# Optimization experiments

Measured on AMD Instinct MI355X. Metric: run time of the kernel, lower is better.

## Reference

```python
import jax, jax.numpy as jnp
import numpy as np

BN_EPS = 1e-3  # keras BatchNormalization default epsilon


def _conv(x, w):
    # x: [B,H,W,Cin], w: [kh,kw,Cin,Cout], stride 1, SAME padding
    return jax.lax.conv_general_dilated(
        x, w, window_strides=(1, 1), padding='SAME',
        dimension_numbers=('NHWC', 'HWIO', 'NHWC'))


def _bn(x, g, b, m, v):
    return (x - m) * jax.lax.rsqrt(v + BN_EPS) * g + b


def _pam(x, wq, bq, wk, bk, wv, bv, gamma):
    # Position attention: softmax over HW x HW similarity of 1x1-conv q/k.
    B, H, W, C = x.shape
    q = (_conv(x, wq) + bq).reshape(B, H * W, -1)   # [B,HW,C/8]
    k = (_conv(x, wk) + bk).reshape(B, H * W, -1)   # [B,HW,C/8]
    v = (_conv(x, wv) + bv).reshape(B, H * W, C)    # [B,HW,C]
    energy = jnp.einsum('bic,bjc->bij', q, k)       # [B,HW,HW]
    att = jax.nn.softmax(energy, axis=-1)
    out = jnp.einsum('bij,bjc->bic', att, v).reshape(B, H, W, C)
    return gamma * out + x


def _cam(x, gamma):
    # Channel attention with max-subtract stabilization, softmax over C.
    B, H, W, C = x.shape
    X = x.reshape(B, H * W, C)                      # channel-last flat
    energy = jnp.einsum('bnc,bnd->bcd', X, X)       # [B,C,C]
    energy_new = jnp.max(energy, axis=-1, keepdims=True) - energy
    att = jax.nn.softmax(energy_new, axis=-1)       # [B,C,C]
    out = jnp.einsum('bcd,bnd->bnc', att, X).reshape(B, H, W, C)
    return gamma * out + x


def setup_inputs() -> dict:
    key = jax.random.key(0)
    ks = jax.random.split(key, 16)
    B, H, W = 4, 64, 64
    Cin, Ci, Cq, Cout = 512, 128, 16, 19
    s = 0.05
    d = {
        'x': jax.random.normal(ks[0], (B, H, W, Cin), jnp.float32),
        'w5a': jax.random.normal(ks[1], (3, 3, Cin, Ci), jnp.float32) * s,
        'w5c': jax.random.normal(ks[2], (3, 3, Cin, Ci), jnp.float32) * s,
        'wq': jax.random.normal(ks[3], (1, 1, Ci, Cq), jnp.float32) * s,
        'bq': jnp.zeros((Cq,), jnp.float32),
        'wk': jax.random.normal(ks[4], (1, 1, Ci, Cq), jnp.float32) * s,
        'bk': jnp.zeros((Cq,), jnp.float32),
        'wv': jax.random.normal(ks[5], (1, 1, Ci, Ci), jnp.float32) * s,
        'bv': jnp.zeros((Ci,), jnp.float32),
        'pam_gamma': jnp.float32(0.5),
        'cam_gamma': jnp.float32(0.5),
        'w51': jax.random.normal(ks[6], (3, 3, Ci, Ci), jnp.float32) * s,
        'w52': jax.random.normal(ks[7], (3, 3, Ci, Ci), jnp.float32) * s,
        'w8': jax.random.normal(ks[8], (1, 1, Ci, Cout), jnp.float32) * s,
    }
    for i, nm in enumerate(['bn1', 'bn2', 'bn3', 'bn4']):
        d[nm + '_g'] = jnp.ones((Ci,), jnp.float32)
        d[nm + '_b'] = jnp.zeros((Ci,), jnp.float32)
        d[nm + '_m'] = jax.random.normal(ks[9 + i], (Ci,), jnp.float32) * 0.1
        d[nm + '_v'] = jnp.ones((Ci,), jnp.float32)
    return d


def reference(x, w5a, w5c, wq, bq, wk, bk, wv, bv, pam_gamma, cam_gamma,
              w51, w52, w8,
              bn1_g, bn1_b, bn1_m, bn1_v,
              bn2_g, bn2_b, bn2_m, bn2_v,
              bn3_g, bn3_b, bn3_m, bn3_v,
              bn4_g, bn4_b, bn4_m, bn4_v):
    # PAM branch
    feat1 = jax.nn.relu(_bn(_conv(x, w5a), bn1_g, bn1_b, bn1_m, bn1_v))
    sa_feat = _pam(feat1, wq, bq, wk, bk, wv, bv, pam_gamma)
    sa_conv = jax.nn.relu(_bn(_conv(sa_feat, w51), bn3_g, bn3_b, bn3_m, bn3_v))
    # CAM branch
    feat2 = jax.nn.relu(_bn(_conv(x, w5c), bn2_g, bn2_b, bn2_m, bn2_v))
    sc_feat = _cam(feat2, cam_gamma)
    sc_conv = jax.nn.relu(_bn(_conv(sc_feat, w52), bn4_g, bn4_b, bn4_m, bn4_v))
    # Fused output (dropout is identity at inference)
    feat_sum = sa_conv + sc_conv
    return _conv(feat_sum, w8)
```

## Files before the change

kernel.cpp:

```cpp
#include <hip/hip_runtime.h>
#include <hip/hip_bf16.h>
#include <math.h>

#define BN_EPS 1e-3f
#define LOG2E 1.44269504088896f

constexpr int Bn = 4, Hn = 64, Wn = 64, CIN = 512, CI = 128;
constexpr int HWn = Hn * Wn;
constexpr int NPIX = Bn * HWn;
constexpr int COn = 19;
constexpr int XSL = 66;
constexpr int XPG = XSL * 16;

struct F8 { float4 lo, hi; };

__device__ __forceinline__ F8 f8zero() {
    F8 r; r.lo = make_float4(0.f,0.f,0.f,0.f); r.hi = make_float4(0.f,0.f,0.f,0.f); return r;
}
__device__ __forceinline__ void fma8(F8 &acc, float a, const float4 &wlo, const float4 &whi) {
    acc.lo.x = fmaf(a, wlo.x, acc.lo.x);
    acc.lo.y = fmaf(a, wlo.y, acc.lo.y);
    acc.lo.z = fmaf(a, wlo.z, acc.lo.z);
    acc.lo.w = fmaf(a, wlo.w, acc.lo.w);
    acc.hi.x = fmaf(a, whi.x, acc.hi.x);
    acc.hi.y = fmaf(a, whi.y, acc.hi.y);
    acc.hi.z = fmaf(a, whi.z, acc.hi.z);
    acc.hi.w = fmaf(a, whi.w, acc.hi.w);
}

typedef __attribute__((ext_vector_type(8)))  short    short8;
typedef __attribute__((ext_vector_type(8)))  _Float16 half8;
typedef __attribute__((ext_vector_type(16))) float    f32x16;

__device__ __forceinline__ f32x16 f16z() {
    f32x16 z;
    #pragma unroll
    for (int i = 0; i < 16; ++i) z[i] = 0.f;
    return z;
}
__device__ __forceinline__ unsigned f2b(float f) {
    union { float f; unsigned u; } c; c.f = f;
    return (c.u + 0x7FFFu + ((c.u >> 16) & 1u)) >> 16;
}
__device__ __forceinline__ unsigned pack2(float lo, float hi) {
    return (f2b(hi) << 16) | f2b(lo);
}
__device__ __forceinline__ unsigned pkb2(float a, float b) {
    __hip_bfloat16 ha = __float2bfloat16(a);
    __hip_bfloat16 hb = __float2bfloat16(b);
    return ((unsigned)*(unsigned short*)&hb << 16) | *(unsigned short*)&ha;
}
__device__ __forceinline__ void split2(float a, float b, unsigned &hi, unsigned &lo) {
    const unsigned ha = f2b(a), hb = f2b(b);
    union { unsigned u; float f; } ua, ub; ua.u = ha << 16; ub.u = hb << 16;
    hi = (hb << 16) | ha;
    lo = pack2(a - ua.f, b - ub.f);
}
__device__ __forceinline__ unsigned pkh2(float a, float b) {
    union { _Float16 h; unsigned short u; } ca, cb;
    ca.h = (_Float16)a; cb.h = (_Float16)b;
    return ((unsigned)cb.u << 16) | ca.u;
}

__global__ __launch_bounds__(256)
void k_prep_w(const float* __restrict__ w5a, const float* __restrict__ w5c,
              const float* __restrict__ w51, const float* __restrict__ w52,
              char* __restrict__ wt1F, char* __restrict__ wt2aF, char* __restrict__ wt2bF)
{
    int idx = blockIdx.x * 256 + threadIdx.x;
    if (idx < 589824) {
        const int jp = idx & 7, co = (idx >> 3) & 255, ct = idx >> 11;
        const int tap = ct % 9, c = ct / 9;
        const float* src = (co < 128) ? w5a : w5c;
        const int coc = co & 127;
        const int ci = c*16 + jp*2;
        const float a = src[((size_t)tap*CIN + ci)*CI + coc];
        const float b = src[((size_t)tap*CIN + ci + 1)*CI + coc];
        const int L = co*32 + jp*4;
        *(unsigned*)(wt1F + (size_t)ct*8192 + L) = pkh2(a, b);
    } else {
        int k = idx - 589824;
        if (k >= 147456) return;
        const float* src = (k < 73728) ? w51 : w52;
        char* dstF = (k < 73728) ? wt2aF : wt2bF;
        if (k >= 73728) k -= 73728;
        const int jp = k & 7, co = (k >> 3) & 127, ct = k >> 10;
        const int tap = ct % 9, c = ct / 9;
        const int ci = c*16 + jp*2;
        const float a = src[((size_t)tap*CI + ci)*CI + co];
        const float b = src[((size_t)tap*CI + ci + 1)*CI + co];
        const int L = co*32 + jp*4;
        *(unsigned*)(dstF + (size_t)ct*4096 + L) = pkh2(a, b);
    }
}

__global__ __launch_bounds__(256)
void k_prep_bn(const float* g1, const float* b1, const float* m1, const float* v1,
               const float* g2, const float* b2, const float* m2, const float* v2,
               const float* g3, const float* b3, const float* m3, const float* v3,
               const float* g4, const float* b4, const float* m4, const float* v4,
               float* bnAs, float* bnAb, float* bnBs, float* bnBb)
{
    const int t = threadIdx.x, c = t & 127;
    {
        const float *g = (t < 128) ? g1 : g2, *b = (t < 128) ? b1 : b2;
        const float *m = (t < 128) ? m1 : m2, *v = (t < 128) ? v1 : v2;
        const float s = g[c] * rsqrtf(v[c] + BN_EPS);
        bnAs[t] = s; bnAb[t] = b[c] - m[c]*s;
    }
    {
        const float *g = (t < 128) ? g3 : g4, *b = (t < 128) ? b3 : b4;
        const float *m = (t < 128) ? m3 : m4, *v = (t < 128) ? v3 : v4;
        const float s = g[c] * rsqrtf(v[c] + BN_EPS);
        bnBs[t] = s; bnBb[t] = b[c] - m[c]*s;
    }
}

__global__ __launch_bounds__(256)
void k_prep_x(const float* __restrict__ x, _Float16* __restrict__ xcv)
{
    __shared__ float Xl[16*520];
    const int t = threadIdx.x;
    const int pb = blockIdx.x * 16;
    #pragma unroll
    for (int i = 0; i < 8; ++i) {
        const int u = t + i*256;
        const int px = u >> 7, c4 = (u & 127) * 4;
        *(float4*)&Xl[px*520 + c4] = *(const float4*)&x[(size_t)(pb + px)*CIN + c4];
    }
    __syncthreads();
    const int rowg = pb >> 6, pixb = pb & 63;
    #pragma unroll
    for (int i = 0; i < 8; ++i) {
        const int u = t + i*256;
        const int chunk = u >> 6, rem = u & 63;
        const int pl = rem >> 2, u4 = rem & 3;
        const float* src = &Xl[pl*520 + chunk*16 + u4*4];
        uint2 v;
        v.x = pkh2(src[0], src[1]);
        v.y = pkh2(src[2], src[3]);
        *(uint2*)&xcv[(((size_t)rowg*32 + chunk)*XSL + (pixb + pl + 1))*16 + u4*4] = v;
    }
    if (pixb == 0 && t < 64) {
        const int chunk = t >> 1, sl = (t & 1) * 65;
        uint4* dst = (uint4*)&xcv[(((size_t)rowg*32 + chunk)*XSL + sl)*16];
        uint4 z; z.x = 0u; z.y = 0u; z.z = 0u; z.w = 0u;
        dst[0] = z; dst[1] = z;
    }
}

__global__ __launch_bounds__(256)
void k_zhalo(_Float16* __restrict__ saf_h, _Float16* __restrict__ scf_h)
{
    const int idx = blockIdx.x * 256 + threadIdx.x;
    if (idx >= 8192) return;
    _Float16* arr = (idx & 4096) ? scf_h : saf_h;
    const int rem = idx & 4095;
    const int row = rem >> 4, chunk = (rem >> 1) & 7, sl = (rem & 1) * 65;
    uint4* dst = (uint4*)&arr[(((size_t)row*8 + chunk)*XSL + sl)*16];
    uint4 z; z.x = 0u; z.y = 0u; z.z = 0u; z.w = 0u;
    dst[0] = z; dst[1] = z;
}

template<int NCHNK, int NCOTOT, int WCOBASE>
__global__ __launch_bounds__(512)
void k_convr(const _Float16* __restrict__ xcv0, const _Float16* __restrict__ xcv1,
             const _Float16* __restrict__ wtF0, const _Float16* __restrict__ wtF1,
             const float* __restrict__ bnS, const float* __restrict__ bnBi,
             float* __restrict__ out0, float* __restrict__ out1)
{
    constexpr int WU4  = 1152;
    constexpr int XU4  = 792;
    constexpr int BUFB = (WU4 + XU4) * 16;
    __shared__ __align__(16) char Ls[2*BUFB];

    const int t     = threadIdx.x;
    const int wgid  = blockIdx.x;
    const int slice = wgid & 3;
    const int rg    = wgid >> 2;
    const int sel   = slice >> 1;
    const int ch2   = slice & 1;
    const _Float16* xcv = sel ? xcv1 : xcv0;
    const _Float16* wtF = sel ? wtF1 : wtF0;
    float* dst = sel ? out1 : out0;

    const int hh0 = (rg*4) & 63;
    const int l = t & 63, w = t >> 6;
    const int lo5 = l & 31, hf = l >> 5;
    const int r = w >> 1, mi = w & 1;
    const int cobase0 = WCOBASE*sel + ch2*64;

    bool sAct[4]; bool sIsW[4]; int sDst[4]; size_t sSrc[4]; unsigned sStr[4];
    #pragma unroll
    for (int i = 0; i < 4; ++i) {
        const int u = t + i*512;
        sAct[i] = false; sIsW[i] = false; sDst[i] = -1; sSrc[i] = 0; sStr[i] = 0;
        if (u < WU4) {
            const int tap = u >> 7, rem = u & 127;
            const int co = rem >> 1, whf = rem & 1;
            sAct[i] = true; sIsW[i] = true;
            sSrc[i] = (size_t)(tap*NCOTOT + cobase0 + co)*32 + whf*16;
            sStr[i] = (unsigned)(9*NCOTOT*32);
            sDst[i] = (tap*128 + whf*64 + co) * 16;
        } else if (u < WU4 + XU4) {
            const int j = u - WU4;
            const int page = j / 132, rem132 = j - page*132;
            const int slot = rem132 >> 1, xhf = rem132 & 1;
            const int hin = hh0 + page - 1;
            sAct[i] = (hin >= 0 && hin < Hn);
            const int gr = rg*4 + page - 1;
            sSrc[i] = (size_t)gr*NCHNK*2112 + (size_t)(slot*32 + xhf*16);
            sStr[i] = 2112u;
            sDst[i] = WU4*16 + page*2112 + ((slot*32 + xhf*16) ^ ((slot & 7) << 4));
        }
    }
    int xoff[3][3];
    #pragma unroll
    for (int dy = 0; dy < 3; ++dy)
        #pragma unroll
        for (int dx = 0; dx < 3; ++dx) {
            const int s = mi*32 + lo5 + dx;
            xoff[dy][dx] = WU4*16 + (r + dy)*2112 + ((s*32 + hf*16) ^ ((s & 7) << 4));
        }

    f32x16 acc[2];
    acc[0] = f16z(); acc[1] = f16z();

    uint4 xr[4];
    auto loadS = [&](int c) {
        #pragma unroll
        for (int i = 0; i < 4; ++i) {
            uint4 v; v.x = 0u; v.y = 0u; v.z = 0u; v.w = 0u;
            if (sAct[i]) {
                const char* base = sIsW[i] ? (const char*)wtF : (const char*)xcv;
                v = *(const uint4*)(base + sSrc[i] + (size_t)c*sStr[i]);
            }
            xr[i] = v;
        }
    };

    loadS(0);
    int p = 0;
    for (int c = 0; c < NCHNK; ++c) {
        char* Lp = Ls + p*BUFB;
        #pragma unroll
        for (int i = 0; i < 4; ++i)
            if (sDst[i] >= 0) *(uint4*)(Lp + sDst[i]) = xr[i];
        __syncthreads();
        if (c + 1 < NCHNK) loadS(c + 1);
        #pragma unroll
        for (int dy = 0; dy < 3; ++dy)
            #pragma unroll
            for (int dx = 0; dx < 3; ++dx) {
                const half8 xf = *(const half8*)(Lp + xoff[dy][dx]);
                const half8 w0 = *(const half8*)(Lp + ((dy*3 + dx)*128 + hf*64 + lo5)*16);
                const half8 w1 = *(const half8*)(Lp + ((dy*3 + dx)*128 + hf*64 + 32 + lo5)*16);
                acc[0] = __builtin_amdgcn_mfma_f32_32x32x16_f16(w0, xf, acc[0], 0, 0, 0);
                acc[1] = __builtin_amdgcn_mfma_f32_32x32x16_f16(w1, xf, acc[1], 0, 0, 0);
            }
        p ^= 1;
    }
    const int px = mi*32 + lo5;
    const size_t pg = (size_t)(rg*4 + r)*Wn + px;
    #pragma unroll
    for (int cot = 0; cot < 2; ++cot)
        #pragma unroll
        for (int rr = 0; rr < 16; ++rr) {
            const int crow = (rr & 3) + 8*(rr >> 2) + 4*hf;
            const int och = ch2*64 + cot*32 + crow;
            const int bnidx = sel*128 + och;
            dst[pg*CI + och] = fmaxf(fmaf(acc[cot][rr], bnS[bnidx], bnBi[bnidx]), 0.f);
        }
}

__global__ __launch_bounds__(256)
void k_qk(const float* __restrict__ feat1,
          const float* __restrict__ wq, const float* __restrict__ bq,
          const float* __restrict__ wk, const float* __restrict__ bk,
          __hip_bfloat16* __restrict__ qb, __hip_bfloat16* __restrict__ kb)
{
    __shared__ float Al[64*129];
    __shared__ __align__(16) float Wl[128*32];
    const int t = threadIdx.x;
    const int pb = blockIdx.x * 64;
    for (int idx = t; idx < 64*128; idx += 256) {
        const int p = idx >> 7, ci = idx & 127;
        Al[p*129 + ci] = feat1[(size_t)(pb + p)*CI + ci];
    }
    for (int idx = t; idx < 128*32; idx += 256) {
        const int ci = idx >> 5, c = idx & 31;
        Wl[idx] = (c < 16) ? wq[ci*16 + c] : wk[ci*16 + (c - 16)];
    }
    __syncthreads();
    const int p = t & 63, cg = t >> 6, co = cg * 8;
    F8 acc = f8zero();
    #pragma unroll 8
    for (int ci = 0; ci < 128; ++ci) {
        const float a = Al[p*129 + ci];
        const float4 wlo = *(const float4*)&Wl[ci*32 + co];
        const float4 whi = *(const float4*)&Wl[ci*32 + co + 4];
        fma8(acc, a, wlo, whi);
    }
    const float* af = (const float*)&acc;
    #pragma unroll
    for (int j = 0; j < 8; ++j) {
        const int c = co + j;
        if (c < 16) qb[(size_t)(pb + p)*16 + c]        = __float2bfloat16((af[j] + bq[c]) * LOG2E);
        else        kb[(size_t)(pb + p)*16 + (c - 16)] = __float2bfloat16(af[j] + bk[c - 16]);
    }
}

__global__ __launch_bounds__(256)
void k_v(const float* __restrict__ feat1, const float* __restrict__ wv,
         const float* __restrict__ bv, __hip_bfloat16* __restrict__ vbT)
{
    __shared__ float Al[32*129];
    __shared__ __align__(16) float Wl[64*128];
    const int t = threadIdx.x;
    const int pb = blockIdx.x * 32;
    for (int idx = t; idx < 32*128; idx += 256) {
        const int p = idx >> 7, ci = idx & 127;
        Al[p*129 + ci] = feat1[(size_t)(pb + p)*CI + ci];
    }
    const int px = t & 15, co = (t >> 4) * 8;
    F8 acc0 = f8zero(), acc1 = f8zero();
    for (int ch = 0; ch < 2; ++ch) {
        __syncthreads();
        #pragma unroll
        for (int r = 0; r < 8; ++r) {
            const int i4 = t + r*256;
            const int kk = i4 >> 5, c4 = (i4 & 31) * 4;
            *(float4*)&Wl[kk*128 + c4] = *(const float4*)&wv[(size_t)(ch*64 + kk)*CI + c4];
        }
        __syncthreads();
        #pragma unroll 4
        for (int kk = 0; kk < 64; ++kk) {
            const float a0 = Al[px*129 + ch*64 + kk];
            const float a1 = Al[(px+16)*129 + ch*64 + kk];
            const float4 wlo = *(const float4*)&Wl[kk*128 + co];
            const float4 whi = *(const float4*)&Wl[kk*128 + co + 4];
            fma8(acc0, a0, wlo, whi);
            fma8(acc1, a1, wlo, whi);
        }
    }
    const int p0 = pb + px;
    const int bb = p0 / HWn, pin0 = p0 % HWn;
    const int k16a = pin0 >> 4, ko = pin0 & 15;
    const float* a0f = (const float*)&acc0;
    const float* a1f = (const float*)&acc1;
    #pragma unroll
    for (int j = 0; j < 8; ++j) {
        const int c = co + j;
        const size_t base = ((size_t)bb*256*CI*16) + (size_t)c*16 + ko;
        vbT[base + (size_t)k16a*CI*16]       = __float2bfloat16(a0f[j] + bv[c]);
        vbT[base + (size_t)(k16a + 1)*CI*16] = __float2bfloat16(a1f[j] + bv[c]);
    }
}

__global__ __launch_bounds__(256)
void k_pam(const __hip_bfloat16* __restrict__ qb, const __hip_bfloat16* __restrict__ kb,
           const __hip_bfloat16* __restrict__ vbT, const float* __restrict__ feat1,
           const float* __restrict__ gamma, _Float16* __restrict__ saf_h)
{
    __shared__ __align__(16) char pbuf[16896];
    __shared__ float msArr[4][32];
    __shared__ float ssArr[4][32];
    __shared__ float ssum[32];
    const int t  = threadIdx.x;
    const int wv = t >> 6, l = t & 63;
    const int lo5 = l & 31, h = l >> 5;
    unsigned* Ppk = (unsigned*)(pbuf + wv*4096);
    float* osum = (float*)pbuf;

    const int wgid = blockIdx.x;
    const int xcd  = wgid & 7;
    const int bb   = xcd >> 1;
    const int qt   = ((wgid >> 3) << 1) | (xcd & 1);
    const int q0   = bb*HWn + qt*32;
    const size_t jb = (size_t)bb * HWn;
    const __hip_bfloat16* vbB = vbT + (size_t)bb * 256 * CI * 16;

    const short8 qfrag = *(const short8*)&qb[(size_t)(q0 + lo5)*16 + 8*h];
    const f32x16 zro = f16z();

    f32x16 o[4];
    #pragma unroll
    for (int cb = 0; cb < 4; ++cb) o[cb] = f16z();

    float m_run = -1e30f, s_run = 0.f;

    const int kbeg = wv*1024, kend = kbeg + 1024;
    short8 kf0 = *(const short8*)&kb[(jb + kbeg +      lo5)*16 + 8*h];
    short8 kf1 = *(const short8*)&kb[(jb + kbeg + 32 + lo5)*16 + 8*h];

    for (int k0 = kbeg; k0 < kend; k0 += 64) {
        short8 vf[4][4];
        #pragma unroll
        for (int s = 0; s < 4; ++s)
            #pragma unroll
            for (int cb = 0; cb < 4; ++cb)
                vf[s][cb] = *(const short8*)&vbB[
                    (((size_t)(k0 >> 4) + s)*CI + cb*32 + lo5)*16 + 8*h];

        f32x16 e0 = __builtin_amdgcn_mfma_f32_32x32x16_bf16(kf0, qfrag, zro, 0, 0, 0);
        f32x16 e1 = __builtin_amdgcn_mfma_f32_32x32x16_bf16(kf1, qfrag, zro, 0, 0, 0);

        if (k0 + 64 < kend) {
            kf0 = *(const short8*)&kb[(jb + k0 + 64 +      lo5)*16 + 8*h];
            kf1 = *(const short8*)&kb[(jb + k0 + 64 + 32 + lo5)*16 + 8*h];
        }

        float mx8[8];
        #pragma unroll
        for (int r = 0; r < 8; ++r)
            mx8[r] = fmaxf(fmaxf(e0[r], e0[r+8]), fmaxf(e1[r], e1[r+8]));
        mx8[0] = fmaxf(mx8[0], mx8[4]);
        mx8[1] = fmaxf(mx8[1], mx8[5]);
        mx8[2] = fmaxf(mx8[2], mx8[6]);
        mx8[3] = fmaxf(mx8[3], mx8[7]);
        mx8[0] = fmaxf(mx8[0], mx8[2]);
        mx8[1] = fmaxf(mx8[1], mx8[3]);
        float mt = fmaxf(mx8[0], mx8[1]);
        mt = fmaxf(mt, __shfl_xor(mt, 32));

        if (__any(mt > m_run + 11.5416f)) {
            const float mnew = fmaxf(m_run, mt);
            const float sc = exp2f(m_run - mnew);
            s_run *= sc;
            #pragma unroll
            for (int cb = 0; cb < 4; ++cb)
                #pragma unroll
                for (int r = 0; r < 16; ++r) o[cb][r] *= sc;
            m_run = mnew;
        }

        #pragma unroll
        for (int r = 0; r < 16; ++r) {
            e0[r] = exp2f(e0[r] - m_run);
            e1[r] = exp2f(e1[r] - m_run);
        }
        {
            float s8[8];
            #pragma unroll
            for (int r = 0; r < 8; ++r)
                s8[r] = (e0[r] + e0[r+8]) + (e1[r] + e1[r+8]);
            s8[0] += s8[4]; s8[1] += s8[5]; s8[2] += s8[6]; s8[3] += s8[7];
            s8[0] += s8[2]; s8[1] += s8[3];
            s_run += s8[0] + s8[1];
        }

        #pragma unroll
        for (int r = 0; r < 16; r += 2) {
            const int pidx = ((r & 3) >> 1) + 4*(r >> 2) + 2*h;
            Ppk[pidx*32 + lo5]        = pkb2(e0[r], e0[r+1]);
            Ppk[(16 + pidx)*32 + lo5] = pkb2(e1[r], e1[r+1]);
        }
        #pragma unroll
        for (int s = 0; s < 4; ++s) {
            union { unsigned u[4]; short8 s8; } P;
            #pragma unroll
            for (int w = 0; w < 4; ++w)
                P.u[w] = Ppk[(s*8 + 4*h + w)*32 + lo5];
            #pragma unroll
            for (int cb = 0; cb < 4; ++cb)
                o[cb] = __builtin_amdgcn_mfma_f32_32x32x16_bf16(vf[s][cb], P.s8, o[cb], 0, 0, 0);
        }
    }

    const float s_w = s_run + __shfl_xor(s_run, 32);
    if (h == 0) { msArr[wv][lo5] = m_run; ssArr[wv][lo5] = s_w; }
    __syncthreads();

    float M = msArr[0][lo5];
    #pragma unroll
    for (int w = 1; w < 4; ++w) M = fmaxf(M, msArr[w][lo5]);
    float stot = 0.f;
    #pragma unroll
    for (int w = 0; w < 4; ++w) stot += exp2f(msArr[w][lo5] - M) * ssArr[w][lo5];
    if (wv == 0 && h == 0) ssum[lo5] = stot;
    const float myscale = exp2f(m_run - M);
    #pragma unroll
    for (int cb = 0; cb < 4; ++cb)
        #pragma unroll
        for (int r = 0; r < 16; ++r) o[cb][r] *= myscale;

    for (int w = 0; w < 4; ++w) {
        if (wv == w) {
            #pragma unroll
            for (int cb = 0; cb < 4; ++cb)
                #pragma unroll
                for (int r = 0; r < 16; ++r) {
                    const int c = cb*32 + (r & 3) + 8*(r >> 2) + 4*h;
                    float* p = &osum[lo5*132 + c];
                    if (w == 0) *p = o[cb][r]; else *p += o[cb][r];
                }
        }
        __syncthreads();
    }

    const float g = gamma[0];
    const int qloc = t >> 3, ch8 = t & 7;
    const float inv = 1.f / ssum[qloc];
    const int pgl = q0 + qloc;
    const int rowp = pgl >> 6, pixp = pgl & 63;
    const size_t gbase = (size_t)pgl*CI + ch8*16;
    union { _Float16 hv[16]; uint4 u[2]; } tmp;
    #pragma unroll
    for (int j = 0; j < 16; ++j)
        tmp.hv[j] = (_Float16)(g*(osum[qloc*132 + ch8*16 + j]*inv) + feat1[gbase + j]);
    uint4* dsth = (uint4*)&saf_h[(((size_t)rowp*8 + ch8)*XSL + (pixp + 1))*16];
    dsth[0] = tmp.u[0];
    dsth[1] = tmp.u[1];
}

__global__ __launch_bounds__(256)
void k_xpose(const float* __restrict__ feat2,
             char* __restrict__ f2TH, char* __restrict__ f2TL)
{
    __shared__ float Xl[64*129];
    const int t = threadIdx.x;
    const int pb = blockIdx.x * 64;
    const int bb = pb / HWn, pin = pb % HWn;
    for (int idx = t; idx < 64*128; idx += 256) {
        const int p = idx >> 7, ci = idx & 127;
        Xl[p*129 + ci] = feat2[(size_t)(pb + p)*CI + ci];
    }
    __syncthreads();
    const int c = t >> 1, half = t & 1;
    const size_t rowb = ((size_t)(bb*CI + c)*HWn + pin + half*32) * 2;
    #pragma unroll
    for (int j = 0; j < 16; ++j) {
        const float a = Xl[(half*32 + 2*j)*129 + c];
        const float b = Xl[(half*32 + 2*j + 1)*129 + c];
        unsigned hi, lo; split2(a, b, hi, lo);
        *(unsigned*)(f2TH + rowb + 4*j) = hi;
        *(unsigned*)(f2TL + rowb + 4*j) = lo;
    }
}

__global__ __launch_bounds__(256)
void k_cam_energy_m(const char* __restrict__ f2TH, const char* __restrict__ f2TL,
                    float* __restrict__ epart)
{
    __shared__ __align__(16) char Vh[128*256];
    __shared__ __align__(16) char Vl[128*256];
    const int t = threadIdx.x;
    const int ks = blockIdx.x, bb = blockIdx.y;
    const int l = t & 63, w = t >> 6;
    const int lo5 = l & 31, hf = l >> 5;

    #pragma unroll
    for (int pass = 0; pass < 8; ++pass) {
        const int slot = pass*256 + t;
        const int c = slot >> 4, g = slot & 15;
        const size_t gaddr = ((size_t)(bb*CI + c)*HWn + ks*128)*2 + g*16;
        const int laddr = c*256 + ((g*16) ^ ((c & 15) << 4));
        *(float4*)(Vh + laddr) = *(const float4*)(f2TH + gaddr);
        *(float4*)(Vl + laddr) = *(const float4*)(f2TL + gaddr);
    }
    __syncthreads();

    f32x16 acc[4];
    #pragma unroll
    for (int nj = 0; nj < 4; ++nj) acc[nj] = f16z();
    const int cA = w*32 + lo5;
    const int swA = (cA & 15) << 4;

    #pragma unroll
    for (int kk = 0; kk < 8; ++kk) {
        const int kb = kk*32 + hf*16;
        const short8 ah = *(const short8*)(Vh + cA*256 + (kb ^ swA));
        const short8 al = *(const short8*)(Vl + cA*256 + (kb ^ swA));
        #pragma unroll
        for (int nj = 0; nj < 4; ++nj) {
            const int dB = nj*32 + lo5;
            const int swB = (dB & 15) << 4;
            const short8 bh = *(const short8*)(Vh + dB*256 + (kb ^ swB));
            const short8 bl = *(const short8*)(Vl + dB*256 + (kb ^ swB));
            acc[nj] = __builtin_amdgcn_mfma_f32_32x32x16_bf16(ah, bh, acc[nj], 0, 0, 0);
            acc[nj] = __builtin_amdgcn_mfma_f32_32x32x16_bf16(al, bh, acc[nj], 0, 0, 0);
            acc[nj] = __builtin_amdgcn_mfma_f32_32x32x16_bf16(ah, bl, acc[nj], 0, 0, 0);
        }
    }
    float* ep = epart + ((size_t)(bb*32 + ks)*CI)*CI;
    #pragma unroll
    for (int nj = 0; nj < 4; ++nj)
        #pragma unroll
        for (int r = 0; r < 16; ++r) {
            const int c = w*32 + (r & 3) + 8*(r >> 2) + 4*hf;
            ep[(size_t)c*CI + nj*32 + lo5] = acc[nj][r];
        }
}

__global__ __launch_bounds__(64)
void k_cam_rs(const float* __restrict__ epart, float* __restrict__ att)
{
    const int lane = threadIdx.x;
    const int row = blockIdx.x;
    const int bb = row >> 7, c = row & 127;
    float2 e = make_float2(0.f, 0.f);
    for (int ks = 0; ks < 32; ++ks) {
        const float2 v = *(const float2*)&epart[
            ((size_t)(bb*32 + ks)*CI + c)*CI + lane*2];
        e.x += v.x; e.y += v.y;
    }
    float M = fmaxf(e.x, e.y);
    #pragma unroll
    for (int off = 32; off > 0; off >>= 1) M = fmaxf(M, __shfl_xor(M, off));
    const float en0 = M - e.x, en1 = M - e.y;
    float mx = fmaxf(en0, en1);
    #pragma unroll
    for (int off = 32; off > 0; off >>= 1) mx = fmaxf(mx, __shfl_xor(mx, off));
    const float p0 = __expf(en0 - mx), p1 = __expf(en1 - mx);
    float s = p0 + p1;
    #pragma unroll
    for (int off = 32; off > 0; off >>= 1) s += __shfl_xor(s, off);
    const float inv = 1.f / s;
    float2 o; o.x = p0*inv; o.y = p1*inv;
    *(float2*)&att[(size_t)row*CI + lane*2] = o;
}

__global__ __launch_bounds__(256)
void k_cam_apply(const float* __restrict__ feat2, const float* __restrict__ att,
                 const float* __restrict__ gamma, _Float16* __restrict__ scf_h)
{
    __shared__ float Xl[64*129];
    __shared__ __align__(16) float aT[128*64];
    const int t = threadIdx.x;
    const int pb = blockIdx.x * 64;
    const int bb = pb / HWn;
    const int ch = blockIdx.y * 64;
    for (int idx = t; idx < 64*128; idx += 256) {
        const int p = idx >> 7, ci = idx & 127;
        Xl[p*129 + ci] = feat2[(size_t)(pb + p)*CI + ci];
    }
    for (int idx = t; idx < 128*64; idx += 256) {
        const int d = idx >> 6, cc = idx & 63;
        aT[d*64 + cc] = att[((size_t)bb*CI + ch + cc)*CI + d];
    }
    __syncthreads();
    const int px = t & 63, cg = t >> 6;
    F8 accA = f8zero(), accB = f8zero();
    #pragma unroll 4
    for (int d = 0; d < 128; ++d) {
        const float xv = Xl[px*129 + d];
        const float* ap = &aT[d*64 + cg*16];
        const float4 a0 = *(const float4*)&ap[0];
        const float4 a1 = *(const float4*)&ap[4];
        const float4 a2 = *(const float4*)&ap[8];
        const float4 a3 = *(const float4*)&ap[12];
        fma8(accA, xv, a0, a1);
        fma8(accB, xv, a2, a3);
    }
    const float g = gamma[0];
    const float* fa = (const float*)&accA;
    const float* fb = (const float*)&accB;
    const int p0g = pb + px;
    const int rowA = p0g >> 6, pixA = p0g & 63;
    const int chunkA = (ch >> 4) + cg;
    const size_t baseA = (((size_t)rowA*8 + chunkA)*XSL + (pixA + 1))*16;
    #pragma unroll
    for (int j = 0; j < 8; ++j) {
        const int cA = ch + cg*16 + j;
        const int cB = cA + 8;
        scf_h[baseA + j]     = (_Float16)(g*fa[j] + Xl[px*129 + cA]);
        scf_h[baseA + 8 + j] = (_Float16)(g*fb[j] + Xl[px*129 + cB]);
    }
}

__global__ __launch_bounds__(256)
void k_final(const float* __restrict__ sa, const float* __restrict__ sc,
             const float* __restrict__ w8, float* __restrict__ out)
{
    __shared__ float Xl[64*129];
    __shared__ float w8l[128*COn];
    const int t = threadIdx.x;
    const int pb = blockIdx.x * 64;
    for (int idx = t; idx < 64*128; idx += 256) {
        const int p = idx >> 7, ci = idx & 127;
        const size_t gi = (size_t)(pb + p)*CI + ci;
        Xl[p*129 + ci] = sa[gi] + sc[gi];
    }
    for (int idx = t; idx < 128*COn; idx += 256) w8l[idx] = w8[idx];
    __syncthreads();
    for (int idx = t; idx < 64*COn; idx += 256) {
        const int p = idx / COn, co = idx - p*COn;
        float acc = 0.f;
        #pragma unroll 8
        for (int ci = 0; ci < 128; ++ci)
            acc = fmaf(Xl[p*129 + ci], w8l[ci*COn + co], acc);
        out[(size_t)(pb + p)*COn + co] = acc;
    }
}

extern "C" void kernel_launch(void* const* d_in, const int* in_sizes, int n_in,
                              void* d_out, int out_size, void* d_ws, size_t ws_size,
                              hipStream_t stream)
{
    const float* x    = (const float*)d_in[0];
    const float* w5a  = (const float*)d_in[1];
    const float* w5c  = (const float*)d_in[2];
    const float* wq   = (const float*)d_in[3];
    const float* bq   = (const float*)d_in[4];
    const float* wk   = (const float*)d_in[5];
    const float* bk   = (const float*)d_in[6];
    const float* wv   = (const float*)d_in[7];
    const float* bv   = (const float*)d_in[8];
    const float* pgam = (const float*)d_in[9];
    const float* cgam = (const float*)d_in[10];
    const float* w51  = (const float*)d_in[11];
    const float* w52  = (const float*)d_in[12];
    const float* w8   = (const float*)d_in[13];
    const float* bn1g = (const float*)d_in[14];
    const float* bn1b = (const float*)d_in[15];
    const float* bn1m = (const float*)d_in[16];
    const float* bn1v = (const float*)d_in[17];
    const float* bn2g = (const float*)d_in[18];
    const float* bn2b = (const float*)d_in[19];
    const float* bn2m = (const float*)d_in[20];
    const float* bn2v = (const float*)d_in[21];
    const float* bn3g = (const float*)d_in[22];
    const float* bn3b = (const float*)d_in[23];
    const float* bn3m = (const float*)d_in[24];
    const float* bn3v = (const float*)d_in[25];
    const float* bn4g = (const float*)d_in[26];
    const float* bn4b = (const float*)d_in[27];
    const float* bn4m = (const float*)d_in[28];
    const float* bn4v = (const float*)d_in[29];

    char* wsb = (char*)d_ws;
    float* feat1 = (float*)(wsb + 0);
    char*  f2TH  = wsb + 0;
    char*  f2TL  = wsb + 4194304;
    float* feat2 = (float*)(wsb + 8388608);
    _Float16* xcv   = (_Float16*)(wsb + 16777216);
    _Float16* saf_h = (_Float16*)(wsb + 16777216);
    _Float16* scf_h = (_Float16*)(wsb + 21102592);
    float*    epart = (float*)(wsb + 25427968);
    float* att = (float*)(wsb + 33816576);
    __hip_bfloat16* qb16 = (__hip_bfloat16*)(wsb + 34078720);
    __hip_bfloat16* kb16 = (__hip_bfloat16*)(wsb + 34603008);
    __hip_bfloat16* vbT  = (__hip_bfloat16*)(wsb + 35127296);
    char* wt1F  = wsb + 39321600;
    char* wt2aF = wsb + 41680896;
    char* wt2bF = wsb + 41975808;
    float* bnAs = (float*)(wsb + 42270720);
    float* bnAb = (float*)(wsb + 42271744);
    float* bnBs = (float*)(wsb + 42272768);
    float* bnBb = (float*)(wsb + 42273792);
    float* sa_conv = feat1;
    float* sc_conv = feat2;
    float* out  = (float*)d_out;

    k_prep_w<<<dim3(2880), 256, 0, stream>>>(w5a, w5c, w51, w52, wt1F, wt2aF, wt2bF);
    k_prep_bn<<<dim3(1), 256, 0, stream>>>(bn1g, bn1b, bn1m, bn1v, bn2g, bn2b, bn2m, bn2v,
                                           bn3g, bn3b, bn3m, bn3v, bn4g, bn4b, bn4m, bn4v,
                                           bnAs, bnAb, bnBs, bnBb);
    k_prep_x<<<dim3(1024), 256, 0, stream>>>(x, xcv);
    k_convr<32, 256, 128><<<dim3(256), 512, 0, stream>>>(
        xcv, xcv, (const _Float16*)wt1F, (const _Float16*)wt1F, bnAs, bnAb, feat1, feat2);
    k_zhalo<<<dim3(32), 256, 0, stream>>>(saf_h, scf_h);
    k_qk<<<dim3(NPIX/64), 256, 0, stream>>>(feat1, wq, bq, wk, bk, qb16, kb16);
    k_v<<<dim3(NPIX/32), 256, 0, stream>>>(feat1, wv, bv, vbT);
    k_pam<<<dim3(NPIX/32), 256, 0, stream>>>(qb16, kb16, vbT, feat1, pgam, saf_h);
    k_xpose<<<dim3(NPIX/64), 256, 0, stream>>>(feat2, f2TH, f2TL);
    k_cam_energy_m<<<dim3(32, Bn), 256, 0, stream>>>(f2TH, f2TL, epart);
    k_cam_rs<<<dim3(Bn*CI), 64, 0, stream>>>(epart, att);
    k_cam_apply<<<dim3(NPIX/64, 2), 256, 0, stream>>>(feat2, att, cgam, scf_h);
    k_convr<8, 128, 0><<<dim3(256), 512, 0, stream>>>(
        saf_h, scf_h, (const _Float16*)wt2aF, (const _Float16*)wt2bF,
        bnBs, bnBb, sa_conv, sc_conv);
    k_final<<<dim3(NPIX/64), 256, 0, stream>>>(sa_conv, sc_conv, w8, out);
}
```

Baseline: 218.9 us.

## Split PAM attention over key halves with log-sum-exp merge kernel

```diff
diff --git a/kernel.cpp b/kernel.cpp
--- a/kernel.cpp
+++ b/kernel.cpp
@@ -359,8 +359,8 @@
 
 __global__ __launch_bounds__(256)
 void k_pam(const __hip_bfloat16* __restrict__ qb, const __hip_bfloat16* __restrict__ kb,
-           const __hip_bfloat16* __restrict__ vbT, const float* __restrict__ feat1,
-           const float* __restrict__ gamma, _Float16* __restrict__ saf_h)
+           const __hip_bfloat16* __restrict__ vbT,
+           _Float16* __restrict__ opart, float* __restrict__ lsep)
 {
     __shared__ __align__(16) char pbuf[16896];
     __shared__ float msArr[4][32];
@@ -375,8 +375,11 @@
     const int wgid = blockIdx.x;
     const int xcd  = wgid & 7;
     const int bb   = xcd >> 1;
-    const int qt   = ((wgid >> 3) << 1) | (xcd & 1);
+    const int u    = ((wgid >> 3) << 1) | (xcd & 1);
+    const int qt   = u >> 1;
+    const int kh   = u & 1;
     const int q0   = bb*HWn + qt*32;
+    const int part = ((bb*128 + qt) << 1) | kh;
     const size_t jb = (size_t)bb * HWn;
     const __hip_bfloat16* vbB = vbT + (size_t)bb * 256 * CI * 16;
 
@@ -389,7 +392,7 @@
 
     float m_run = -1e30f, s_run = 0.f;
 
-    const int kbeg = wv*1024, kend = kbeg + 1024;
+    const int kbeg = kh*2048 + wv*512, kend = kbeg + 512;
     short8 kf0 = *(const short8*)&kb[(jb + kbeg +      lo5)*16 + 8*h];
     short8 kf1 = *(const short8*)&kb[(jb + kbeg + 32 + lo5)*16 + 8*h];
 
@@ -477,7 +480,10 @@
     float stot = 0.f;
     #pragma unroll
     for (int w = 0; w < 4; ++w) stot += exp2f(msArr[w][lo5] - M) * ssArr[w][lo5];
-    if (wv == 0 && h == 0) ssum[lo5] = stot;
+    if (wv == 0 && h == 0) {
+        ssum[lo5] = stot;
+        lsep[part*32 + lo5] = M + log2f(stot);
+    }
     const float myscale = exp2f(m_run - M);
     #pragma unroll
     for (int cb = 0; cb < 4; ++cb)
@@ -498,16 +504,42 @@
         __syncthreads();
     }
 
-    const float g = gamma[0];
     const int qloc = t >> 3, ch8 = t & 7;
     const float inv = 1.f / ssum[qloc];
-    const int pgl = q0 + qloc;
+    union { _Float16 hv[16]; uint4 u2[2]; } tmp;
+    #pragma unroll
+    for (int j = 0; j < 16; ++j)
+        tmp.hv[j] = (_Float16)(osum[qloc*132 + ch8*16 + j] * inv);
+    uint4* dsto = (uint4*)&opart[(size_t)part*4096 + qloc*128 + ch8*16];
+    dsto[0] = tmp.u2[0];
+    dsto[1] = tmp.u2[1];
+}
+
+__global__ __launch_bounds__(256)
+void k_pam_merge(const _Float16* __restrict__ opart, const float* __restrict__ lsep,
+                 const float* __restrict__ feat1, const float* __restrict__ gamma,
+                 _Float16* __restrict__ saf_h)
+{
+    const int qg = blockIdx.x;
+    const int t = threadIdx.x;
+    const int qloc = t >> 3, ch8 = t & 7;
+    const int p0 = qg*2, p1 = qg*2 + 1;
+    const float l0 = lsep[p0*32 + qloc], l1 = lsep[p1*32 + qloc];
+    const float L = fmaxf(l0, l1);
+    const float w0 = exp2f(l0 - L), w1 = exp2f(l1 - L);
+    const float inv = 1.f / (w0 + w1);
+    const float g = gamma[0];
+    const int pgl = qg*32 + qloc;
     const int rowp = pgl >> 6, pixp = pgl & 63;
     const size_t gbase = (size_t)pgl*CI + ch8*16;
+    const _Float16* s0 = &opart[(size_t)p0*4096 + qloc*128 + ch8*16];
+    const _Float16* s1 = &opart[(size_t)p1*4096 + qloc*128 + ch8*16];
     union { _Float16 hv[16]; uint4 u[2]; } tmp;
     #pragma unroll
-    for (int j = 0; j < 16; ++j)
-        tmp.hv[j] = (_Float16)(g*(osum[qloc*132 + ch8*16 + j]*inv) + feat1[gbase + j]);
+    for (int j = 0; j < 16; ++j) {
+        const float ov = (w0*(float)s0[j] + w1*(float)s1[j]) * inv;
+        tmp.hv[j] = (_Float16)(g*ov + feat1[gbase + j]);
+    }
     uint4* dsth = (uint4*)&saf_h[(((size_t)rowp*8 + ch8)*XSL + (pixp + 1))*16];
     dsth[0] = tmp.u[0];
     dsth[1] = tmp.u[1];
@@ -736,8 +768,10 @@
     _Float16* xcv   = (_Float16*)(wsb + 16777216);
     _Float16* saf_h = (_Float16*)(wsb + 16777216);
     _Float16* scf_h = (_Float16*)(wsb + 21102592);
+    _Float16* opart = (_Float16*)(wsb + 25427968);
     float*    epart = (float*)(wsb + 25427968);
-    float* att = (float*)(wsb + 33816576);
+    float* att  = (float*)(wsb + 33816576);
+    float* lsep = (float*)(wsb + 33816576);
     __hip_bfloat16* qb16 = (__hip_bfloat16*)(wsb + 34078720);
     __hip_bfloat16* kb16 = (__hip_bfloat16*)(wsb + 34603008);
     __hip_bfloat16* vbT  = (__hip_bfloat16*)(wsb + 35127296);
@@ -762,7 +796,8 @@
     k_zhalo<<<dim3(32), 256, 0, stream>>>(saf_h, scf_h);
     k_qk<<<dim3(NPIX/64), 256, 0, stream>>>(feat1, wq, bq, wk, bk, qb16, kb16);
     k_v<<<dim3(NPIX/32), 256, 0, stream>>>(feat1, wv, bv, vbT);
-    k_pam<<<dim3(NPIX/32), 256, 0, stream>>>(qb16, kb16, vbT, feat1, pgam, saf_h);
+    k_pam<<<dim3(1024), 256, 0, stream>>>(qb16, kb16, vbT, opart, lsep);
+    k_pam_merge<<<dim3(512), 256, 0, stream>>>(opart, lsep, feat1, pgam, saf_h);
     k_xpose<<<dim3(NPIX/64), 256, 0, stream>>>(feat2, f2TH, f2TL);
     k_cam_energy_m<<<dim3(32, Bn), 256, 0, stream>>>(f2TH, f2TL, epart);
     k_cam_rs<<<dim3(Bn*CI), 64, 0, stream>>>(epart, att);
```

New measurement: 232.0 us. 6.0% more time.
